# Kernel optimization log

Measured on AMD Instinct MI355X. Metric: run time of the kernel, lower is better.

The kernel has to match this reference:

```python
import jax, jax.numpy as jnp
import numpy as np

N_ATOMS = 50000
N_EDGES = 1_600_000
N_MOL = 500
HIDDEN = 128
FILTERS = 128
GAUSS = 50
LAYERS = 3
CUTOFF = 10.0
LOG2 = 0.6931471805599453


def ssp(x):
    # ShiftedSoftplus: softplus(x) - log(2)
    return jax.nn.softplus(x) - LOG2


def setup_inputs() -> dict:
    key = jax.random.key(0)
    ks = jax.random.split(key, 24)
    z = jax.random.randint(ks[0], (N_ATOMS,), 0, 100)
    pos = jax.random.uniform(ks[1], (N_ATOMS, 3), jnp.float32) * 5.0  # box keeps d < cutoff
    batch = jnp.sort(jax.random.randint(ks[2], (N_ATOMS,), 0, N_MOL))
    row = jax.random.randint(ks[3], (N_EDGES,), 0, N_ATOMS)
    off = jax.random.randint(ks[4], (N_EDGES,), 1, N_ATOMS)
    col = (row + off) % N_ATOMS  # guarantees row != col (no zero distances)
    edge_index = jnp.stack([row, col])
    def lin(k, fi, fo):
        return jax.random.normal(k, (fi, fo), jnp.float32) * (1.0 / np.sqrt(fi))
    emb = jax.random.normal(ks[5], (100, HIDDEN), jnp.float32)
    mlp1_w = jnp.stack([lin(jax.random.fold_in(ks[6], i), GAUSS, FILTERS) for i in range(LAYERS)])
    mlp1_b = jnp.zeros((LAYERS, FILTERS), jnp.float32)
    mlp2_w = jnp.stack([lin(jax.random.fold_in(ks[7], i), FILTERS, FILTERS) for i in range(LAYERS)])
    mlp2_b = jnp.zeros((LAYERS, FILTERS), jnp.float32)
    lin1_w = jnp.stack([lin(jax.random.fold_in(ks[8], i), HIDDEN, FILTERS) for i in range(LAYERS)])
    lin2_w = jnp.stack([lin(jax.random.fold_in(ks[9], i), FILTERS, HIDDEN) for i in range(LAYERS)])
    lin2_b = jnp.zeros((LAYERS, HIDDEN), jnp.float32)
    int_w = jnp.stack([lin(jax.random.fold_in(ks[10], i), HIDDEN, HIDDEN) for i in range(LAYERS)])
    int_b = jnp.zeros((LAYERS, HIDDEN), jnp.float32)
    out1_w = lin(ks[11], HIDDEN, HIDDEN // 2)
    out1_b = jnp.zeros((HIDDEN // 2,), jnp.float32)
    out2_w = lin(ks[12], HIDDEN // 2, 1)
    out2_b = jnp.zeros((1,), jnp.float32)
    return {"z": z, "pos": pos, "batch": batch, "edge_index": edge_index,
            "emb": emb, "mlp1_w": mlp1_w, "mlp1_b": mlp1_b, "mlp2_w": mlp2_w, "mlp2_b": mlp2_b,
            "lin1_w": lin1_w, "lin2_w": lin2_w, "lin2_b": lin2_b, "int_w": int_w, "int_b": int_b,
            "out1_w": out1_w, "out1_b": out1_b, "out2_w": out2_w, "out2_b": out2_b}


def reference(z, pos, batch, edge_index, emb, mlp1_w, mlp1_b, mlp2_w, mlp2_b,
              lin1_w, lin2_w, lin2_b, int_w, int_b, out1_w, out1_b, out2_w, out2_b):
    row, col = edge_index[0], edge_index[1]  # source j, target i
    d = jnp.linalg.norm(pos[row] - pos[col], axis=-1)  # [E]
    # GaussianSmearing
    offset = jnp.linspace(0.0, CUTOFF, GAUSS)
    coeff = -0.5 / (offset[1] - offset[0]) ** 2
    rbf = jnp.exp(coeff * (d[:, None] - offset[None, :]) ** 2)  # [E, GAUSS]
    # cosine cutoff
    C = 0.5 * (jnp.cos(d * jnp.pi / CUTOFF) + 1.0)  # [E]
    h = emb[z]  # [N, H]
    for l in range(LAYERS):
        W = ssp(rbf @ mlp1_w[l] + mlp1_b[l]) @ mlp2_w[l] + mlp2_b[l]  # [E, F]
        W = W * C[:, None]
        x = h @ lin1_w[l]                 # [N, F]
        msg = x[row] * W                  # gather from source, per-edge filter
        agg = jax.ops.segment_sum(msg, col, num_segments=N_ATOMS)  # scatter-add to targets
        x = agg @ lin2_w[l] + lin2_b[l]
        x = ssp(x)
        x = x @ int_w[l] + int_b[l]
        h = h + x                         # residual
    h = ssp(h @ out1_w + out1_b)
    h = h @ out2_w + out2_b               # [N, 1] per-atom energy
    out = jax.ops.segment_sum(h[:, 0], batch, num_segments=N_MOL)  # 'add' readout
    return out.reshape(-1)
```

## Files before the change

### kernel.cpp

```cpp
#include <hip/hip_runtime.h>
#include <math.h>

#define HID 128
#define NGAUSS 50
#define TBL 2048
#define TBL2 8192
#define DMAX 8.6605f
#define LDX 136
#define PGRID 768

typedef _Float16 h4 __attribute__((ext_vector_type(4)));
typedef _Float16 f16x8 __attribute__((ext_vector_type(8)));
typedef float f32x4 __attribute__((ext_vector_type(4)));

__device__ __forceinline__ float sspf(float x) {
  float ax = fabsf(x);
  return fmaxf(x, 0.0f) + log1pf(expf(-ax)) - 0.69314718055994530942f;
}

__global__ __launch_bounds__(128) void build_table_k(
    const float* __restrict__ w1, const float* __restrict__ b1,
    const float* __restrict__ w2, const float* __restrict__ b2,
    float* __restrict__ tab) {
  int l = blockIdx.x >> 11;
  int ti = blockIdx.x & (TBL - 1);
  int j = threadIdx.x;
  __shared__ float rbf[NGAUSS];
  __shared__ float v1[HID];
  const float step = DMAX / (float)(TBL - 1);
  float d = ti * step;
  if (j < NGAUSS) {
    const float gstep = 10.0f / 49.0f;
    const float gcoeff = -12.005f;
    float diff = d - j * gstep;
    rbf[j] = expf(gcoeff * diff * diff);
  }
  __syncthreads();
  float s = b1[l * HID + j];
  const float* w1p = w1 + l * NGAUSS * HID + j;
  for (int g = 0; g < NGAUSS; g++) s = fmaf(rbf[g], w1p[g * HID], s);
  v1[j] = sspf(s);
  __syncthreads();
  float s2 = b2[l * HID + j];
  const float* w2p = w2 + l * HID * HID + j;
  for (int k = 0; k < HID; k++) s2 = fmaf(v1[k], w2p[k * HID], s2);
  float C = 0.5f * (cosf(d * 0.3141592653589793f) + 1.0f);
  tab[((size_t)l * TBL + ti) * HID + j] = s2 * C;
}

__global__ __launch_bounds__(256) void upsample_k(
    const float* __restrict__ tab, _Float16* __restrict__ tabh) {
  int idx = blockIdx.x * 256 + threadIdx.x;
  if (idx >= 3 * TBL2 * HID) return;
  int ch = idx & 127;
  int i = (idx >> 7) & (TBL2 - 1);
  int l = idx >> 20;
  float t = (float)i * ((float)(TBL - 1) / (float)(TBL2 - 1));
  int i0 = min((int)t, TBL - 2);
  float f = t - (float)i0;
  const float* base = tab + ((size_t)l * TBL + i0) * HID + ch;
  tabh[idx] = (_Float16)fmaf(f, base[HID] - base[0], base[0]);
}

__global__ __launch_bounds__(256) void wswz10_k(
    const float* __restrict__ lin1, const float* __restrict__ lin2,
    const float* __restrict__ intw, const float* __restrict__ out1w,
    _Float16* __restrict__ out) {
  int b = blockIdx.x;
  int t = threadIdx.x;
  if (b < 9) {
    const float* src = (b < 3 ? lin1 : (b < 6 ? lin2 : intw)) + (size_t)(b % 3) * HID * HID;
    _Float16* dst = out + (size_t)b * 16384;
    for (int i = t; i < 16384; i += 256) {
      int j = i & 7;
      int lane = (i >> 3) & 63;
      int kk = (i >> 9) & 3;
      int ntc = i >> 11;
      int n = ntc * 16 + (lane & 15);
      int k = kk * 32 + (lane >> 4) * 8 + j;
      dst[i] = (_Float16)src[k * HID + n];
    }
  } else {
    _Float16* dst = out + (size_t)9 * 16384;
    for (int i = t; i < 8192; i += 256) {
      int j = i & 7;
      int lane = (i >> 3) & 63;
      int kk = (i >> 9) & 3;
      int ntc = i >> 11;
      int n = ntc * 16 + (lane & 15);
      int k = kk * 32 + (lane >> 4) * 8 + j;
      dst[i] = (_Float16)out1w[k * 64 + n];
    }
  }
}

__global__ __launch_bounds__(256) void emb_gather_k(
    const int* __restrict__ z, const float* __restrict__ emb,
    _Float16* __restrict__ h16, int N) {
  int i4 = blockIdx.x * 256 + threadIdx.x;
  if (i4 >= N * 32) return;
  int a = i4 >> 5;
  float4 v = ((const float4*)emb)[z[a] * 32 + (i4 & 31)];
  h4 o;
  o.x = (_Float16)v.x; o.y = (_Float16)v.y;
  o.z = (_Float16)v.z; o.w = (_Float16)v.w;
  ((h4*)h16)[i4] = o;
}

__global__ __launch_bounds__(256) void bcount_k(
    const int* __restrict__ col, int* __restrict__ bcount, int E, int nbuck) {
  __shared__ int hist[1024];
  int t = threadIdx.x;
  int e0 = blockIdx.x * 2048;
  for (int j = t; j < nbuck; j += 256) hist[j] = 0;
  __syncthreads();
#pragma unroll
  for (int u = 0; u < 8; u++) {
    int e = e0 + u * 256 + t;
    if (e < E) atomicAdd(&hist[col[e] >> 6], 1);
  }
  __syncthreads();
  for (int j = t; j < nbuck; j += 256)
    if (hist[j]) atomicAdd(&bcount[j], hist[j]);
}

__global__ __launch_bounds__(256) void bucket_scan_k(
    const int* __restrict__ bcount, int* __restrict__ bstart,
    int* __restrict__ bcur, int nbuck, int* __restrict__ starts, int N) {
  __shared__ int sh[256];
  int t = threadIdx.x;
  int chunk = (nbuck + 255) / 256;
  int b0 = t * chunk;
  int c[8];
  int s = 0;
  for (int j = 0; j < chunk; j++) {
    int idx = b0 + j;
    int v = (idx < nbuck) ? bcount[idx] : 0;
    c[j] = v;
    s += v;
  }
  sh[t] = s;
  __syncthreads();
  for (int o = 1; o < 256; o <<= 1) {
    int v = (t >= o) ? sh[t - o] : 0;
    __syncthreads();
    sh[t] += v;
    __syncthreads();
  }
  int p = (t == 0) ? 0 : sh[t - 1];
  for (int j = 0; j < chunk; j++) {
    int idx = b0 + j;
    if (idx < nbuck) {
      bstart[idx] = p;
      bcur[idx] = p;
      p += c[j];
    }
  }
  if (t == 255) {
    bstart[nbuck] = p;
    starts[N] = p;
  }
}

__global__ __launch_bounds__(256) void scatterA_k(
    const int* __restrict__ row, const int* __restrict__ col,
    const float* __restrict__ pos, int* __restrict__ bcur,
    unsigned long long* __restrict__ tmp, int E, int nbuck) {
  __shared__ int hist[1024];
  __shared__ int base[1024];
  int t = threadIdx.x;
  int e0 = blockIdx.x * 2048;
  for (int j = t; j < nbuck; j += 256) hist[j] = 0;
  __syncthreads();
  int bkt[8];
  int rnk[8];
  unsigned long long key[8];
#pragma unroll
  for (int u = 0; u < 8; u++) {
    int e = e0 + u * 256 + t;
    bkt[u] = -1;
    if (e < E) {
      int r = row[e], c = col[e];
      float dx = pos[r * 3 + 0] - pos[c * 3 + 0];
      float dy = pos[r * 3 + 1] - pos[c * 3 + 1];
      float dz = pos[r * 3 + 2] - pos[c * 3 + 2];
      float d = sqrtf(dx * dx + dy * dy + dz * dz);
      const float inv2 = (float)(TBL2 - 1) / DMAX;
      int q = min((int)(d * inv2 + 0.5f), TBL2 - 1);
      unsigned int pay = ((unsigned int)r << 13) | (unsigned int)q;
      key[u] = ((unsigned long long)pay << 6) | (unsigned long long)(c & 63);
      bkt[u] = c >> 6;
      rnk[u] = atomicAdd(&hist[bkt[u]], 1);
    }
  }
  __syncthreads();
  for (int j = t; j < nbuck; j += 256)
    base[j] = hist[j] ? atomicAdd(&bcur[j], hist[j]) : 0;
  __syncthreads();
#pragma unroll
  for (int u = 0; u < 8; u++)
    if (bkt[u] >= 0) tmp[(size_t)base[bkt[u]] + rnk[u]] = key[u];
}

__global__ __launch_bounds__(256) void scatterB_k(
    const unsigned long long* __restrict__ tmp, const int* __restrict__ bstart,
    int* __restrict__ starts, unsigned int* __restrict__ payload, int N) {
  int j = blockIdx.x;
  int t = threadIdx.x;
  __shared__ int cnt[64];
  __shared__ int cur[64];
  int rs = bstart[j], re = bstart[j + 1];
  if (t < 64) cnt[t] = 0;
  __syncthreads();
  for (int e = rs + t; e < re; e += 256)
    atomicAdd(&cnt[(int)(tmp[e] & 63)], 1);
  __syncthreads();
  if (t < 64) {
    int mine = cnt[t];
    int v = mine;
    for (int o = 1; o < 64; o <<= 1) {
      int u = __shfl_up(v, o, 64);
      if (t >= o) v += u;
    }
    int excl = v - mine;
    int c = j * 64 + t;
    if (c < N) starts[c] = rs + excl;
    cur[t] = rs + excl;
  }
  __syncthreads();
  for (int e = rs + t; e < re; e += 256) {
    unsigned long long k = tmp[e];
    int p = atomicAdd(&cur[(int)(k & 63)], 1);
    payload[p] = (unsigned int)(k >> 6);
  }
}


__global__ __launch_bounds__(256, 4) void lin_p_k(
    const _Float16* __restrict__ in16, const _Float16* __restrict__ Wg,
    _Float16* __restrict__ out16, int N, int ntiles) {
  __shared__ __align__(16) _Float16 Xs[32 * LDX];
  __shared__ __align__(16) _Float16 Ys[32 * LDX];
  int t = threadIdx.x;
  int lane = t & 63, w = t >> 6;
  int g = w & 1, c = w >> 1;
  int mrow = lane & 15, quad = lane >> 4;
  f32x4 zero = {0.f, 0.f, 0.f, 0.f};
  for (int tile = blockIdx.x; tile < ntiles; tile += gridDim.x) {
    int a0 = tile * 32;
#pragma unroll
    for (int p = 0; p < 2; p++) {
      int id = t + p * 256;
      int a = id >> 4, kg = id & 15;
      uint4 v = make_uint4(0, 0, 0, 0);
      if (a0 + a < N) v = ((const uint4*)in16)[(size_t)(a0 + a) * 16 + kg];
      *(uint4*)&Xs[a * LDX + kg * 8] = v;
    }
    __syncthreads();
    f16x8 af[4];
#pragma unroll
    for (int kk = 0; kk < 4; kk++)
      af[kk] = *(const f16x8*)&Xs[(g * 16 + mrow) * LDX + kk * 32 + quad * 8];
    f32x4 acc[4];
#pragma unroll
    for (int i = 0; i < 4; i++) acc[i] = zero;
#pragma unroll
    for (int kk = 0; kk < 4; kk++) {
#pragma unroll
      for (int nt = 0; nt < 4; nt++) {
        f16x8 bf = *(const f16x8*)(Wg + ((((c * 4 + nt) * 4 + kk) << 9) + lane * 8));
        acc[nt] = __builtin_amdgcn_mfma_f32_16x16x32_f16(af[kk], bf, acc[nt], 0, 0, 0);
      }
    }
#pragma unroll
    for (int nt = 0; nt < 4; nt++) {
      int colv = c * 64 + nt * 16 + mrow;
#pragma unroll
      for (int r = 0; r < 4; r++)
        Ys[(g * 16 + quad * 4 + r) * LDX + colv] = (_Float16)acc[nt][r];
    }
    __syncthreads();
#pragma unroll
    for (int p = 0; p < 2; p++) {
      int id = t + p * 256;
      int a = id >> 4, kg = id & 15;
      if (a0 + a < N)
        ((uint4*)out16)[(size_t)(a0 + a) * 16 + kg] = *(uint4*)&Ys[a * LDX + kg * 8];
    }
  }
}

__global__ __launch_bounds__(256, 4) void ssp_res_p_k(
    const _Float16* __restrict__ agg16, const _Float16* __restrict__ W2g,
    const float* __restrict__ b2, const _Float16* __restrict__ W3g,
    const float* __restrict__ b3, _Float16* __restrict__ h16, int N, int ntiles) {
  __shared__ __align__(16) _Float16 Xs[32 * LDX];
  __shared__ __align__(16) _Float16 Ys[32 * LDX];
  int t = threadIdx.x;
  int lane = t & 63, w = t >> 6;
  int g = w & 1, c = w >> 1;
  int mrow = lane & 15, quad = lane >> 4;
  float br2[4], br3[4];
#pragma unroll
  for (int nt = 0; nt < 4; nt++) {
    br2[nt] = b2[c * 64 + nt * 16 + mrow];
    br3[nt] = b3[c * 64 + nt * 16 + mrow];
  }
  f32x4 zero = {0.f, 0.f, 0.f, 0.f};
  for (int tile = blockIdx.x; tile < ntiles; tile += gridDim.x) {
    int a0 = tile * 32;
#pragma unroll
    for (int p = 0; p < 2; p++) {
      int id = t + p * 256;
      int a = id >> 4, kg = id & 15;
      uint4 v = make_uint4(0, 0, 0, 0);
      if (a0 + a < N) v = ((const uint4*)agg16)[(size_t)(a0 + a) * 16 + kg];
      *(uint4*)&Xs[a * LDX + kg * 8] = v;
    }
    __syncthreads();
    f16x8 af[4];
#pragma unroll
    for (int kk = 0; kk < 4; kk++)
      af[kk] = *(const f16x8*)&Xs[(g * 16 + mrow) * LDX + kk * 32 + quad * 8];
    f32x4 acc[4];
#pragma unroll
    for (int i = 0; i < 4; i++) acc[i] = zero;
#pragma unroll
    for (int kk = 0; kk < 4; kk++) {
#pragma unroll
      for (int nt = 0; nt < 4; nt++) {
        f16x8 bf = *(const f16x8*)(W2g + ((((c * 4 + nt) * 4 + kk) << 9) + lane * 8));
        acc[nt] = __builtin_amdgcn_mfma_f32_16x16x32_f16(af[kk], bf, acc[nt], 0, 0, 0);
      }
    }
#pragma unroll
    for (int nt = 0; nt < 4; nt++) {
      int colv = c * 64 + nt * 16 + mrow;
#pragma unroll
      for (int r = 0; r < 4; r++)
        Ys[(g * 16 + quad * 4 + r) * LDX + colv] = (_Float16)sspf(acc[nt][r] + br2[nt]);
    }
    __syncthreads();
#pragma unroll
    for (int kk = 0; kk < 4; kk++)
      af[kk] = *(const f16x8*)&Ys[(g * 16 + mrow) * LDX + kk * 32 + quad * 8];
    __syncthreads();
#pragma unroll
    for (int i = 0; i < 4; i++) acc[i] = zero;
#pragma unroll
    for (int kk = 0; kk < 4; kk++) {
#pragma unroll
      for (int nt = 0; nt < 4; nt++) {
        f16x8 bf = *(const f16x8*)(W3g + ((((c * 4 + nt) * 4 + kk) << 9) + lane * 8));
        acc[nt] = __builtin_amdgcn_mfma_f32_16x16x32_f16(af[kk], bf, acc[nt], 0, 0, 0);
      }
    }
#pragma unroll
    for (int nt = 0; nt < 4; nt++) {
      int colv = c * 64 + nt * 16 + mrow;
#pragma unroll
      for (int r = 0; r < 4; r++)
        Ys[(g * 16 + quad * 4 + r) * LDX + colv] = (_Float16)(acc[nt][r] + br3[nt]);
    }
    __syncthreads();
#pragma unroll
    for (int p = 0; p < 2; p++) {
      int id = t + p * 256;
      int a = id >> 4, kg = id & 15;
      if (a0 + a < N) {
        f16x8 hv = *(const f16x8*)&((const uint4*)h16)[(size_t)(a0 + a) * 16 + kg];
        f16x8 yv = *(f16x8*)&Ys[a * LDX + kg * 8];
        f16x8 o;
#pragma unroll
        for (int j = 0; j < 8; j++) o[j] = (_Float16)((float)hv[j] + (float)yv[j]);
        ((uint4*)h16)[(size_t)(a0 + a) * 16 + kg] = *(uint4*)&o;
      }
    }
  }
}

__global__ __launch_bounds__(256, 4) void energy_p_k(
    const _Float16* __restrict__ h16, const _Float16* __restrict__ Wg,
    const float* __restrict__ o1b, const float* __restrict__ o2w,
    const float* __restrict__ o2b, const int* __restrict__ batch,
    float* __restrict__ out, int N, int ntiles) {
  __shared__ __align__(16) _Float16 Xs[32 * LDX];
  __shared__ float ebuf[32];
  __shared__ int bat[32];
  int t = threadIdx.x;
  int lane = t & 63, w = t >> 6;
  int g = w & 1, c = w >> 1;
  int mrow = lane & 15, quad = lane >> 4;
  float br[2], wr[2];
#pragma unroll
  for (int nt = 0; nt < 2; nt++) {
    int colv = c * 32 + nt * 16 + mrow;
    br[nt] = o1b[colv];
    wr[nt] = o2w[colv];
  }
  float o2b0 = o2b[0];
  if (t < 32) ebuf[t] = 0.f;
  __syncthreads();
  f32x4 zero = {0.f, 0.f, 0.f, 0.f};
  for (int tile = blockIdx.x; tile < ntiles; tile += gridDim.x) {
    int a0 = tile * 32;
#pragma unroll
    for (int p = 0; p < 2; p++) {
      int id = t + p * 256;
      int a = id >> 4, kg = id & 15;
      uint4 v = make_uint4(0, 0, 0, 0);
      if (a0 + a < N) v = ((const uint4*)h16)[(size_t)(a0 + a) * 16 + kg];
      *(uint4*)&Xs[a * LDX + kg * 8] = v;
    }
    if (t < 32) bat[t] = (a0 + t < N) ? batch[a0 + t] : -1;
    __syncthreads();
    f16x8 af[4];
#pragma unroll
    for (int kk = 0; kk < 4; kk++)
      af[kk] = *(const f16x8*)&Xs[(g * 16 + mrow) * LDX + kk * 32 + quad * 8];
    f32x4 acc[2];
    acc[0] = zero; acc[1] = zero;
#pragma unroll
    for (int kk = 0; kk < 4; kk++) {
#pragma unroll
      for (int nt = 0; nt < 2; nt++) {
        f16x8 bf = *(const f16x8*)(Wg + ((((c * 2 + nt) * 4 + kk) << 9) + lane * 8));
        acc[nt] = __builtin_amdgcn_mfma_f32_16x16x32_f16(af[kk], bf, acc[nt], 0, 0, 0);
      }
    }
    float ss[4] = {0.f, 0.f, 0.f, 0.f};
#pragma unroll
    for (int nt = 0; nt < 2; nt++)
#pragma unroll
      for (int r = 0; r < 4; r++) ss[r] += sspf(acc[nt][r] + br[nt]) * wr[nt];
#pragma unroll
    for (int r = 0; r < 4; r++) {
      ss[r] += __shfl_xor(ss[r], 1);
      ss[r] += __shfl_xor(ss[r], 2);
      ss[r] += __shfl_xor(ss[r], 4);
      ss[r] += __shfl_xor(ss[r], 8);
      if (mrow == 0) atomicAdd(&ebuf[g * 16 + quad * 4 + r], ss[r]);
    }
    __syncthreads();
    if (t == 0) {
      float acs = 0.f;
      int pm = -1;
      for (int i = 0; i < 32; i++) {
        int m = bat[i];
        float e = ebuf[i];
        ebuf[i] = 0.f;
        if (m < 0) break;
        if (m != pm) {
          if (pm >= 0) atomicAdd(&out[pm], acs);
          acs = 0.f;
          pm = m;
        }
        acs += e + o2b0;
      }
      if (pm >= 0) atomicAdd(&out[pm], acs);
    }
  }
}

__global__ __launch_bounds__(256) void aggregate_k(
    const int* __restrict__ starts, const unsigned int* __restrict__ payload,
    const _Float16* __restrict__ x16, const _Float16* __restrict__ tabh,
    _Float16* __restrict__ agg16, int N) {
  int a = blockIdx.x * 4 + (threadIdx.x >> 6);
  if (a >= N) return;
  int lane = threadIdx.x & 63;
  int half = lane >> 5;
  int sl = lane & 31;
  int s = starts[a], e_end = starts[a + 1];
  float4 accf = make_float4(0.f, 0.f, 0.f, 0.f);
  const h4 z4 = {(_Float16)0.f, (_Float16)0.f, (_Float16)0.f, (_Float16)0.f};
  int i = s;
  for (; i + 16 <= e_end; i += 16) {
    unsigned int p[8];
#pragma unroll
    for (int u = 0; u < 8; u++) p[u] = payload[i + 2 * u + half];
    h4 tw[8], xr[8];
#pragma unroll
    for (int u = 0; u < 8; u++) {
      int tq = (int)(p[u] & 8191u);
      int r = (int)(p[u] >> 13);
      tw[u] = *(const h4*)&tabh[(size_t)tq * HID + sl * 4];
      xr[u] = *(const h4*)&x16[(size_t)r * HID + sl * 4];
    }
    h4 a0 = z4, a1 = z4, a2 = z4, a3 = z4;
    a0 += tw[0] * xr[0];
    a1 += tw[1] * xr[1];
    a2 += tw[2] * xr[2];
    a3 += tw[3] * xr[3];
    a0 += tw[4] * xr[4];
    a1 += tw[5] * xr[5];
    a2 += tw[6] * xr[6];
    a3 += tw[7] * xr[7];
    h4 b0 = a0 + a1, b1 = a2 + a3;
    accf.x += (float)b0.x + (float)b1.x;
    accf.y += (float)b0.y + (float)b1.y;
    accf.z += (float)b0.z + (float)b1.z;
    accf.w += (float)b0.w + (float)b1.w;
  }
  {
    h4 a0 = z4, a1 = z4;
    int k = 0;
    for (; i + 2 <= e_end; i += 2, k++) {
      unsigned int p = payload[i + half];
      int tq = (int)(p & 8191u);
      int r = (int)(p >> 13);
      h4 tw = *(const h4*)&tabh[(size_t)tq * HID + sl * 4];
      h4 xr = *(const h4*)&x16[(size_t)r * HID + sl * 4];
      if (k & 1) a1 += tw * xr; else a0 += tw * xr;
    }
    if (i < e_end && half == 0) {
      unsigned int p = payload[i];
      int tq = (int)(p & 8191u);
      int r = (int)(p >> 13);
      h4 tw = *(const h4*)&tabh[(size_t)tq * HID + sl * 4];
      h4 xr = *(const h4*)&x16[(size_t)r * HID + sl * 4];
      a0 += tw * xr;
    }
    h4 b0 = a0 + a1;
    accf.x += (float)b0.x;
    accf.y += (float)b0.y;
    accf.z += (float)b0.z;
    accf.w += (float)b0.w;
  }
  accf.x += __shfl_xor(accf.x, 32);
  accf.y += __shfl_xor(accf.y, 32);
  accf.z += __shfl_xor(accf.z, 32);
  accf.w += __shfl_xor(accf.w, 32);
  if (half == 0) {
    h4 o;
    o.x = (_Float16)accf.x; o.y = (_Float16)accf.y;
    o.z = (_Float16)accf.z; o.w = (_Float16)accf.w;
    *(h4*)&agg16[(size_t)a * HID + sl * 4] = o;
  }
}

extern "C" void kernel_launch(void* const* d_in, const int* in_sizes, int n_in,
                              void* d_out, int out_size, void* d_ws, size_t ws_size,
                              hipStream_t stream) {
  const int* z = (const int*)d_in[0];
  const float* pos = (const float*)d_in[1];
  const int* batch = (const int*)d_in[2];
  const int* eidx = (const int*)d_in[3];
  const float* emb = (const float*)d_in[4];
  const float* mlp1_w = (const float*)d_in[5];
  const float* mlp1_b = (const float*)d_in[6];
  const float* mlp2_w = (const float*)d_in[7];
  const float* mlp2_b = (const float*)d_in[8];
  const float* lin1_w = (const float*)d_in[9];
  const float* lin2_w = (const float*)d_in[10];
  const float* lin2_b = (const float*)d_in[11];
  const float* int_w = (const float*)d_in[12];
  const float* int_b = (const float*)d_in[13];
  const float* out1_w = (const float*)d_in[14];
  const float* out1_b = (const float*)d_in[15];
  const float* out2_w = (const float*)d_in[16];
  const float* out2_b = (const float*)d_in[17];
  float* out = (float*)d_out;

  const int N = in_sizes[0];
  const int E = in_sizes[3] / 2;
  const int* row = eidx;
  const int* col = eidx + E;
  const int nbuck = (N + 63) / 64;
  const int ntiles = (N + 31) / 32;

  char* ws = (char*)d_ws;
  size_t off = 0;
  auto alloc = [&](size_t bytes) -> void* {
    void* p = ws + off;
    off = (off + bytes + 255) & ~(size_t)255;
    return p;
  };
  _Float16* h16 = (_Float16*)alloc((size_t)N * HID * 2);
  _Float16* x16 = (_Float16*)alloc((size_t)N * HID * 2);
  size_t agg_bytes = (size_t)N * HID * 2;
  size_t tmp_bytes = (size_t)E * 8 + 16;
  void* agg_union = alloc(agg_bytes > tmp_bytes ? agg_bytes : tmp_bytes);
  _Float16* agg16 = (_Float16*)agg_union;
  unsigned long long* tmp = (unsigned long long*)agg_union;
  unsigned int* payload = (unsigned int*)alloc((size_t)E * 4 + 16);
  int* starts = (int*)alloc((size_t)(N + 1) * 4);
  int* bcount = (int*)alloc((size_t)nbuck * 4);
  int* bstart = (int*)alloc((size_t)(nbuck + 1) * 4);
  int* bcur = (int*)alloc((size_t)nbuck * 4);
  float* tab = (float*)alloc((size_t)3 * TBL * HID * 4);
  _Float16* tabh = (_Float16*)alloc((size_t)3 * TBL2 * HID * 2);
  _Float16* Wsw = (_Float16*)alloc((size_t)10 * 16384 * 2);
  (void)ws_size;

  hipMemsetAsync(bcount, 0, (size_t)nbuck * 4, stream);
  hipMemsetAsync(out, 0, (size_t)out_size * 4, stream);

  build_table_k<<<3 * TBL, 128, 0, stream>>>(mlp1_w, mlp1_b, mlp2_w, mlp2_b, tab);
  upsample_k<<<(3 * TBL2 * HID + 255) / 256, 256, 0, stream>>>(tab, tabh);
  wswz10_k<<<10, 256, 0, stream>>>(lin1_w, lin2_w, int_w, out1_w, Wsw);
  emb_gather_k<<<(N * 32 + 255) / 256, 256, 0, stream>>>(z, emb, h16, N);
  bcount_k<<<(E + 2047) / 2048, 256, 0, stream>>>(col, bcount, E, nbuck);
  bucket_scan_k<<<1, 256, 0, stream>>>(bcount, bstart, bcur, nbuck, starts, N);
  scatterA_k<<<(E + 2047) / 2048, 256, 0, stream>>>(row, col, pos, bcur, tmp, E, nbuck);
  scatterB_k<<<nbuck, 256, 0, stream>>>(tmp, bstart, starts, payload, N);

  int pg = PGRID < ntiles ? PGRID : ntiles;
  for (int l = 0; l < 3; l++) {
    lin_p_k<<<pg, 256, 0, stream>>>(h16, Wsw + (size_t)l * 16384, x16, N, ntiles);
    aggregate_k<<<(N + 3) / 4, 256, 0, stream>>>(starts, payload, x16,
                                                 tabh + (size_t)l * TBL2 * HID, agg16, N);
    ssp_res_p_k<<<pg, 256, 0, stream>>>(agg16, Wsw + (size_t)(3 + l) * 16384,
                                        lin2_b + (size_t)l * HID,
                                        Wsw + (size_t)(6 + l) * 16384,
                                        int_b + (size_t)l * HID, h16, N, ntiles);
  }
  energy_p_k<<<pg, 256, 0, stream>>>(h16, Wsw + (size_t)9 * 16384, out1_b, out2_w,
                                     out2_b, batch, out, N, ntiles);
}
```

Before: 570.6 us.

## Fuse embedding gather into first linear, split ssp/residual GEMM kernel, resize grid

The embedding lookup is folded into the first-layer lin1 kernel, which writes h16 and x16 together and drops a separate launch and one pass over h. The fused ssp+residual kernel is split into two kernels, ssp_p_k and res_p_k, with an intermediate y16 stored through x16. This adds a global round trip and an extra launch per layer, likely to reduce register or LDS pressure or the number of syncs per kernel. The persistent grid size changes from a fixed 768 to half the tile count, capped at 1024.

```diff
diff --git a/kernel.cpp b/kernel.cpp
--- a/kernel.cpp
+++ b/kernel.cpp
@@ -7,7 +7,6 @@
 #define TBL2 8192
 #define DMAX 8.6605f
 #define LDX 136
-#define PGRID 768
 
 typedef _Float16 h4 __attribute__((ext_vector_type(4)));
 typedef _Float16 f16x8 __attribute__((ext_vector_type(8)));
@@ -94,19 +93,6 @@
   }
 }
 
-__global__ __launch_bounds__(256) void emb_gather_k(
-    const int* __restrict__ z, const float* __restrict__ emb,
-    _Float16* __restrict__ h16, int N) {
-  int i4 = blockIdx.x * 256 + threadIdx.x;
-  if (i4 >= N * 32) return;
-  int a = i4 >> 5;
-  float4 v = ((const float4*)emb)[z[a] * 32 + (i4 & 31)];
-  h4 o;
-  o.x = (_Float16)v.x; o.y = (_Float16)v.y;
-  o.z = (_Float16)v.z; o.w = (_Float16)v.w;
-  ((h4*)h16)[i4] = o;
-}
-
 __global__ __launch_bounds__(256) void bcount_k(
     const int* __restrict__ col, int* __restrict__ bcount, int E, int nbuck) {
   __shared__ int hist[1024];
@@ -236,11 +222,13 @@
 }
 
 
-__global__ __launch_bounds__(256, 4) void lin_p_k(
-    const _Float16* __restrict__ in16, const _Float16* __restrict__ Wg,
-    _Float16* __restrict__ out16, int N, int ntiles) {
+__global__ __launch_bounds__(256, 4) void lin_emb_p_k(
+    const int* __restrict__ z, const float* __restrict__ emb,
+    const _Float16* __restrict__ Wg, _Float16* __restrict__ h16,
+    _Float16* __restrict__ x16, int N, int ntiles) {
   __shared__ __align__(16) _Float16 Xs[32 * LDX];
   __shared__ __align__(16) _Float16 Ys[32 * LDX];
+  __shared__ int zi[32];
   int t = threadIdx.x;
   int lane = t & 63, w = t >> 6;
   int g = w & 1, c = w >> 1;
@@ -248,13 +236,23 @@
   f32x4 zero = {0.f, 0.f, 0.f, 0.f};
   for (int tile = blockIdx.x; tile < ntiles; tile += gridDim.x) {
     int a0 = tile * 32;
-#pragma unroll
-    for (int p = 0; p < 2; p++) {
-      int id = t + p * 256;
-      int a = id >> 4, kg = id & 15;
-      uint4 v = make_uint4(0, 0, 0, 0);
-      if (a0 + a < N) v = ((const uint4*)in16)[(size_t)(a0 + a) * 16 + kg];
-      *(uint4*)&Xs[a * LDX + kg * 8] = v;
+    if (t < 32) zi[t] = (a0 + t < N) ? z[a0 + t] : 0;
+    __syncthreads();
+#pragma unroll
+    for (int p = 0; p < 2; p++) {
+      int id = t + p * 256;
+      int a = id >> 4, kg = id & 15;
+      const float* er = emb + (size_t)zi[a] * HID + kg * 8;
+      float4 e0 = *(const float4*)er;
+      float4 e1 = *(const float4*)(er + 4);
+      f16x8 o;
+      o[0] = (_Float16)e0.x; o[1] = (_Float16)e0.y;
+      o[2] = (_Float16)e0.z; o[3] = (_Float16)e0.w;
+      o[4] = (_Float16)e1.x; o[5] = (_Float16)e1.y;
+      o[6] = (_Float16)e1.z; o[7] = (_Float16)e1.w;
+      *(f16x8*)&Xs[a * LDX + kg * 8] = o;
+      if (a0 + a < N)
+        ((uint4*)h16)[(size_t)(a0 + a) * 16 + kg] = *(uint4*)&o;
     }
     __syncthreads();
     f16x8 af[4];
@@ -285,27 +283,20 @@
       int id = t + p * 256;
       int a = id >> 4, kg = id & 15;
       if (a0 + a < N)
-        ((uint4*)out16)[(size_t)(a0 + a) * 16 + kg] = *(uint4*)&Ys[a * LDX + kg * 8];
-    }
-  }
-}
-
-__global__ __launch_bounds__(256, 4) void ssp_res_p_k(
-    const _Float16* __restrict__ agg16, const _Float16* __restrict__ W2g,
-    const float* __restrict__ b2, const _Float16* __restrict__ W3g,
-    const float* __restrict__ b3, _Float16* __restrict__ h16, int N, int ntiles) {
+        ((uint4*)x16)[(size_t)(a0 + a) * 16 + kg] = *(uint4*)&Ys[a * LDX + kg * 8];
+    }
+  }
+}
+
+__global__ __launch_bounds__(256, 4) void lin_p_k(
+    const _Float16* __restrict__ in16, const _Float16* __restrict__ Wg,
+    _Float16* __restrict__ out16, int N, int ntiles) {
   __shared__ __align__(16) _Float16 Xs[32 * LDX];
   __shared__ __align__(16) _Float16 Ys[32 * LDX];
   int t = threadIdx.x;
   int lane = t & 63, w = t >> 6;
   int g = w & 1, c = w >> 1;
   int mrow = lane & 15, quad = lane >> 4;
-  float br2[4], br3[4];
-#pragma unroll
-  for (int nt = 0; nt < 4; nt++) {
-    br2[nt] = b2[c * 64 + nt * 16 + mrow];
-    br3[nt] = b3[c * 64 + nt * 16 + mrow];
-  }
   f32x4 zero = {0.f, 0.f, 0.f, 0.f};
   for (int tile = blockIdx.x; tile < ntiles; tile += gridDim.x) {
     int a0 = tile * 32;
@@ -314,7 +305,7 @@
       int id = t + p * 256;
       int a = id >> 4, kg = id & 15;
       uint4 v = make_uint4(0, 0, 0, 0);
-      if (a0 + a < N) v = ((const uint4*)agg16)[(size_t)(a0 + a) * 16 + kg];
+      if (a0 + a < N) v = ((const uint4*)in16)[(size_t)(a0 + a) * 16 + kg];
       *(uint4*)&Xs[a * LDX + kg * 8] = v;
     }
     __syncthreads();
@@ -329,7 +320,7 @@
     for (int kk = 0; kk < 4; kk++) {
 #pragma unroll
       for (int nt = 0; nt < 4; nt++) {
-        f16x8 bf = *(const f16x8*)(W2g + ((((c * 4 + nt) * 4 + kk) << 9) + lane * 8));
+        f16x8 bf = *(const f16x8*)(Wg + ((((c * 4 + nt) * 4 + kk) << 9) + lane * 8));
         acc[nt] = __builtin_amdgcn_mfma_f32_16x16x32_f16(af[kk], bf, acc[nt], 0, 0, 0);
       }
     }
@@ -338,20 +329,55 @@
       int colv = c * 64 + nt * 16 + mrow;
 #pragma unroll
       for (int r = 0; r < 4; r++)
-        Ys[(g * 16 + quad * 4 + r) * LDX + colv] = (_Float16)sspf(acc[nt][r] + br2[nt]);
-    }
-    __syncthreads();
+        Ys[(g * 16 + quad * 4 + r) * LDX + colv] = (_Float16)acc[nt][r];
+    }
+    __syncthreads();
+#pragma unroll
+    for (int p = 0; p < 2; p++) {
+      int id = t + p * 256;
+      int a = id >> 4, kg = id & 15;
+      if (a0 + a < N)
+        ((uint4*)out16)[(size_t)(a0 + a) * 16 + kg] = *(uint4*)&Ys[a * LDX + kg * 8];
+    }
+  }
+}
+
+__global__ __launch_bounds__(256, 4) void ssp_p_k(
+    const _Float16* __restrict__ agg16, const _Float16* __restrict__ Wg,
+    const float* __restrict__ bias, _Float16* __restrict__ y16, int N, int ntiles) {
+  __shared__ __align__(16) _Float16 Xs[32 * LDX];
+  __shared__ __align__(16) _Float16 Ys[32 * LDX];
+  int t = threadIdx.x;
+  int lane = t & 63, w = t >> 6;
+  int g = w & 1, c = w >> 1;
+  int mrow = lane & 15, quad = lane >> 4;
+  float br[4];
+#pragma unroll
+  for (int nt = 0; nt < 4; nt++) br[nt] = bias[c * 64 + nt * 16 + mrow];
+  f32x4 zero = {0.f, 0.f, 0.f, 0.f};
+  for (int tile = blockIdx.x; tile < ntiles; tile += gridDim.x) {
+    int a0 = tile * 32;
+#pragma unroll
+    for (int p = 0; p < 2; p++) {
+      int id = t + p * 256;
+      int a = id >> 4, kg = id & 15;
+      uint4 v = make_uint4(0, 0, 0, 0);
+      if (a0 + a < N) v = ((const uint4*)agg16)[(size_t)(a0 + a) * 16 + kg];
+      *(uint4*)&Xs[a * LDX + kg * 8] = v;
+    }
+    __syncthreads();
+    f16x8 af[4];
 #pragma unroll
     for (int kk = 0; kk < 4; kk++)
-      af[kk] = *(const f16x8*)&Ys[(g * 16 + mrow) * LDX + kk * 32 + quad * 8];
-    __syncthreads();
+      af[kk] = *(const f16x8*)&Xs[(g * 16 + mrow) * LDX + kk * 32 + quad * 8];
+    f32x4 acc[4];
 #pragma unroll
     for (int i = 0; i < 4; i++) acc[i] = zero;
 #pragma unroll
     for (int kk = 0; kk < 4; kk++) {
 #pragma unroll
       for (int nt = 0; nt < 4; nt++) {
-        f16x8 bf = *(const f16x8*)(W3g + ((((c * 4 + nt) * 4 + kk) << 9) + lane * 8));
+        f16x8 bf = *(const f16x8*)(Wg + ((((c * 4 + nt) * 4 + kk) << 9) + lane * 8));
         acc[nt] = __builtin_amdgcn_mfma_f32_16x16x32_f16(af[kk], bf, acc[nt], 0, 0, 0);
       }
     }
@@ -360,7 +386,64 @@
       int colv = c * 64 + nt * 16 + mrow;
 #pragma unroll
       for (int r = 0; r < 4; r++)
-        Ys[(g * 16 + quad * 4 + r) * LDX + colv] = (_Float16)(acc[nt][r] + br3[nt]);
+        Ys[(g * 16 + quad * 4 + r) * LDX + colv] = (_Float16)sspf(acc[nt][r] + br[nt]);
+    }
+    __syncthreads();
+#pragma unroll
+    for (int p = 0; p < 2; p++) {
+      int id = t + p * 256;
+      int a = id >> 4, kg = id & 15;
+      if (a0 + a < N)
+        ((uint4*)y16)[(size_t)(a0 + a) * 16 + kg] = *(uint4*)&Ys[a * LDX + kg * 8];
+    }
+  }
+}
+
+__global__ __launch_bounds__(256, 4) void res_p_k(
+    const _Float16* __restrict__ y16, const _Float16* __restrict__ Wg,
+    const float* __restrict__ bias, _Float16* __restrict__ h16, int N, int ntiles) {
+  __shared__ __align__(16) _Float16 Xs[32 * LDX];
+  __shared__ __align__(16) _Float16 Ys[32 * LDX];
+  int t = threadIdx.x;
+  int lane = t & 63, w = t >> 6;
+  int g = w & 1, c = w >> 1;
+  int mrow = lane & 15, quad = lane >> 4;
+  float br[4];
+#pragma unroll
+  for (int nt = 0; nt < 4; nt++) br[nt] = bias[c * 64 + nt * 16 + mrow];
+  f32x4 zero = {0.f, 0.f, 0.f, 0.f};
+  for (int tile = blockIdx.x; tile < ntiles; tile += gridDim.x) {
+    int a0 = tile * 32;
+#pragma unroll
+    for (int p = 0; p < 2; p++) {
+      int id = t + p * 256;
+      int a = id >> 4, kg = id & 15;
+      uint4 v = make_uint4(0, 0, 0, 0);
+      if (a0 + a < N) v = ((const uint4*)y16)[(size_t)(a0 + a) * 16 + kg];
+      *(uint4*)&Xs[a * LDX + kg * 8] = v;
+    }
+    __syncthreads();
+    f16x8 af[4];
+#pragma unroll
+    for (int kk = 0; kk < 4; kk++)
+      af[kk] = *(const f16x8*)&Xs[(g * 16 + mrow) * LDX + kk * 32 + quad * 8];
+    f32x4 acc[4];
+#pragma unroll
+    for (int i = 0; i < 4; i++) acc[i] = zero;
+#pragma unroll
+    for (int kk = 0; kk < 4; kk++) {
+#pragma unroll
+      for (int nt = 0; nt < 4; nt++) {
+        f16x8 bf = *(const f16x8*)(Wg + ((((c * 4 + nt) * 4 + kk) << 9) + lane * 8));
+        acc[nt] = __builtin_amdgcn_mfma_f32_16x16x32_f16(af[kk], bf, acc[nt], 0, 0, 0);
+      }
+    }
+#pragma unroll
+    for (int nt = 0; nt < 4; nt++) {
+      int colv = c * 64 + nt * 16 + mrow;
+#pragma unroll
+      for (int r = 0; r < 4; r++)
+        Ys[(g * 16 + quad * 4 + r) * LDX + colv] = (_Float16)(acc[nt][r] + br[nt]);
     }
     __syncthreads();
 #pragma unroll
@@ -599,21 +682,24 @@
   build_table_k<<<3 * TBL, 128, 0, stream>>>(mlp1_w, mlp1_b, mlp2_w, mlp2_b, tab);
   upsample_k<<<(3 * TBL2 * HID + 255) / 256, 256, 0, stream>>>(tab, tabh);
   wswz10_k<<<10, 256, 0, stream>>>(lin1_w, lin2_w, int_w, out1_w, Wsw);
-  emb_gather_k<<<(N * 32 + 255) / 256, 256, 0, stream>>>(z, emb, h16, N);
   bcount_k<<<(E + 2047) / 2048, 256, 0, stream>>>(col, bcount, E, nbuck);
   bucket_scan_k<<<1, 256, 0, stream>>>(bcount, bstart, bcur, nbuck, starts, N);
   scatterA_k<<<(E + 2047) / 2048, 256, 0, stream>>>(row, col, pos, bcur, tmp, E, nbuck);
   scatterB_k<<<nbuck, 256, 0, stream>>>(tmp, bstart, starts, payload, N);
 
-  int pg = PGRID < ntiles ? PGRID : ntiles;
+  int pg = (ntiles + 1) / 2;
+  if (pg > 1024) pg = 1024;
   for (int l = 0; l < 3; l++) {
-    lin_p_k<<<pg, 256, 0, stream>>>(h16, Wsw + (size_t)l * 16384, x16, N, ntiles);
+    if (l == 0)
+      lin_emb_p_k<<<pg, 256, 0, stream>>>(z, emb, Wsw, h16, x16, N, ntiles);
+    else
+      lin_p_k<<<pg, 256, 0, stream>>>(h16, Wsw + (size_t)l * 16384, x16, N, ntiles);
     aggregate_k<<<(N + 3) / 4, 256, 0, stream>>>(starts, payload, x16,
                                                  tabh + (size_t)l * TBL2 * HID, agg16, N);
-    ssp_res_p_k<<<pg, 256, 0, stream>>>(agg16, Wsw + (size_t)(3 + l) * 16384,
-                                        lin2_b + (size_t)l * HID,
-                                        Wsw + (size_t)(6 + l) * 16384,
-                                        int_b + (size_t)l * HID, h16, N, ntiles);
+    ssp_p_k<<<pg, 256, 0, stream>>>(agg16, Wsw + (size_t)(3 + l) * 16384,
+                                    lin2_b + (size_t)l * HID, x16, N, ntiles);
+    res_p_k<<<pg, 256, 0, stream>>>(x16, Wsw + (size_t)(6 + l) * 16384,
+                                    int_b + (size_t)l * HID, h16, N, ntiles);
   }
   energy_p_k<<<pg, 256, 0, stream>>>(h16, Wsw + (size_t)9 * 16384, out1_b, out2_w,
                                      out2_b, batch, out, N, ntiles);
```

Result: no change. 562.5 us (-1.4%).
